# Kernel optimization log

Hardware: AMD Instinct MI355X
Metric: run time of the kernel (lower is better)

Reference implementation:

```python
import jax, jax.numpy as jnp
import numpy as np

B, N, K = 4, 100000, 128
Q_MIN = 0.5
S_B = 1.0
POT_SCALE = 1.0
REP_SCALE = 1.0
BETA_SCALE = 1.0
E_WEIGHT = 1.0
POS_WEIGHT = 1.0
TIME_WEIGHT = 1.0
HUBER_D = 2.0


def setup_inputs() -> dict:
    key = jax.random.key(0)
    ks = jax.random.split(key, 9)
    return {
        "beta": jax.random.uniform(ks[0], (B, N), dtype=jnp.float32),
        "ccoords": jax.random.normal(ks[1], (B, N, 2), dtype=jnp.float32),
        "pred_energy": jax.random.uniform(ks[2], (B, N), dtype=jnp.float32),
        "pred_pos": jax.random.normal(ks[3], (B, N, 2), dtype=jnp.float32),
        "pred_time": jax.random.uniform(ks[4], (B, N), dtype=jnp.float32),
        "t_energy": jax.random.uniform(ks[5], (B, N), dtype=jnp.float32),
        "t_pos": jax.random.normal(ks[6], (B, N, 2), dtype=jnp.float32),
        "t_time": jax.random.uniform(ks[7], (B, N), dtype=jnp.float32),
        "t_idx": jax.random.randint(ks[8], (B, N), 0, K + 1, dtype=jnp.int32),
    }


def _huber(x, d):
    a = jnp.abs(x)
    return jnp.where(a <= d, 0.5 * x * x, d * (a - 0.5 * d))


def _oc_loss(beta, ccoords, pred_energy, pred_pos, pred_time,
             t_energy, t_pos, t_time, t_idx):
    eps = 1e-4
    beta = jnp.clip(beta, eps, 1.0 - eps)
    q = jnp.arctanh(beta) ** 2 + Q_MIN                     # [B,N]

    obj = t_idx - 1                                        # -1 = noise, 0..K-1 = object id
    M = obj[:, :, None] == jnp.arange(K, dtype=jnp.int32)  # [B,N,K] bool membership
    Mf = M.astype(q.dtype)
    obj_exists = jnp.any(M, axis=1)                        # [B,K]
    exf = obj_exists.astype(q.dtype)

    # condensation point per object = member hit with max charge q (segment argmax)
    q_masked = jnp.where(M, q[:, :, None], -1.0)           # [B,N,K]
    alpha = jnp.argmax(q_masked, axis=1)                   # [B,K]
    x_alpha = jnp.take_along_axis(ccoords, alpha[:, :, None], axis=1)  # [B,K,2]
    q_alpha = jnp.take_along_axis(q, alpha, axis=1)        # [B,K]
    beta_alpha = jnp.take_along_axis(beta, alpha, axis=1)  # [B,K]

    # pairwise hit <-> condensation-point distances, [B,N,K]
    diff = ccoords[:, :, None, :] - x_alpha[:, None, :, :]
    dist = jnp.sqrt(jnp.sum(diff * diff, axis=-1) + 1e-12)

    qq = q[:, :, None] * q_alpha[:, None, :] * exf[:, None, :]
    v_att = qq * (dist * dist) * Mf
    v_rep = qq * jax.nn.relu(1.0 - dist) * (1.0 - Mf)
    n_tot = jnp.asarray(B * N, q.dtype)
    L_att = jnp.sum(v_att) / n_tot
    L_rep = jnp.sum(v_rep) / n_tot

    # beta loss: pull condensation-point betas to 1, suppress noise betas
    n_obj = jnp.maximum(jnp.sum(exf), 1.0)
    L_beta_obj = jnp.sum((1.0 - beta_alpha) * exf) / n_obj
    noise = (t_idx == 0).astype(q.dtype)
    L_noise = jnp.sum(beta * noise) / jnp.maximum(jnp.sum(noise), 1.0)
    L_beta = L_beta_obj + S_B * L_noise

    # payload losses, beta-weighted over non-noise hits
    p = (jnp.arctanh(beta) ** 2) * (1.0 - noise)           # [B,N]
    p_sum = jnp.maximum(jnp.sum(p), 1e-6)
    L_energy = jnp.sum(p * _huber(pred_energy - t_energy, HUBER_D)) / p_sum
    L_pos = jnp.sum(p * jnp.sum((pred_pos - t_pos) ** 2, axis=-1)) / p_sum
    L_time = jnp.sum(p * (pred_time - t_time) ** 2) / p_sum

    return (POT_SCALE * L_att + REP_SCALE * L_rep + BETA_SCALE * L_beta
            + E_WEIGHT * L_energy + POS_WEIGHT * L_pos + TIME_WEIGHT * L_time)


def reference(beta, ccoords, pred_energy, pred_pos, pred_time,
              t_energy, t_pos, t_time, t_idx):
    return _oc_loss(beta, ccoords, pred_energy, pred_pos, pred_time,
                    t_energy, t_pos, t_time, t_idx)
```

## Files before the change

kernel.cpp:

```cpp
#include <hip/hip_runtime.h>
#include <math.h>

#define BB 4
#define NN 100000
#define KK 128


__device__ __forceinline__ float clipb(float b) {
    return fminf(fmaxf(b, 1e-4f), 1.0f - 1e-4f);
}

__global__ void k_argmax(const float* __restrict__ beta,
                         const int* __restrict__ tidx,
                         unsigned long long* __restrict__ packed) {
    int b = blockIdx.y;
    __shared__ unsigned long long smax[KK];
    for (int t = threadIdx.x; t < KK; t += blockDim.x) smax[t] = 0ULL;
    __syncthreads();
    const float* betab = beta + b * NN;
    const int*   tib   = tidx + b * NN;
    for (int n = blockIdx.x * blockDim.x + threadIdx.x; n < NN;
         n += gridDim.x * blockDim.x) {
        int obj = tib[n] - 1;
        if (obj >= 0) {
            unsigned hi = __float_as_uint(clipb(betab[n]));
            unsigned long long key = ((unsigned long long)hi << 32) |
                                     (unsigned long long)(0xFFFFFFFFu - (unsigned)n);
            atomicMax(&smax[obj], key);
        }
    }
    __syncthreads();
    for (int t = threadIdx.x; t < KK; t += blockDim.x) {
        unsigned long long v = smax[t];
        if (v) atomicMax(&packed[b * KK + t], v);
    }
}

__global__ void k_gather(const unsigned long long* __restrict__ packed,
                         const float2* __restrict__ cc,
                         float4* __restrict__ sobj,
                         float* __restrict__ acc) {
    int t = blockIdx.x * blockDim.x + threadIdx.x;
    if (t >= BB * KK) return;
    int b = t / KK;
    unsigned long long v = packed[t];
    float4 o = make_float4(0.f, 0.f, 0.f, 0.f);
    if (v) {
        unsigned n = 0xFFFFFFFFu - (unsigned)(v & 0xFFFFFFFFu);
        float ba = __uint_as_float((unsigned)(v >> 32));
        float at = atanhf(ba);
        float2 c = cc[b * NN + (int)n];
        o.x = c.x; o.y = c.y; o.z = at * at + 0.5f; o.w = 1.0f;
        atomicAdd(&acc[8], 1.0f);
        atomicAdd(&acc[9], 1.0f - ba);
    }
    sobj[t] = o;
}

#define HH 2

__global__ void __launch_bounds__(256) k_main(
    const float*  __restrict__ beta, const float2* __restrict__ cc,
    const float*  __restrict__ pe,   const float2* __restrict__ pp,
    const float*  __restrict__ pt,   const float*  __restrict__ te,
    const float2* __restrict__ tp,   const float*  __restrict__ tt,
    const int*    __restrict__ tidx, const float4* __restrict__ sobjg,
    float* __restrict__ acc) {
    int b = blockIdx.y;
    __shared__ float4 sobj[KK];
    __shared__ float sred[4][8];
    for (int t = threadIdx.x; t < KK; t += blockDim.x) sobj[t] = sobjg[b * KK + t];
    __syncthreads();

    float p_att = 0.f, p_rep = 0.f, p_nb = 0.f, p_nc = 0.f;
    float p_ps = 0.f, p_e = 0.f, p_pos = 0.f, p_tm = 0.f;

    int n0 = blockIdx.x * (256 * HH) + threadIdx.x;
    int n1 = n0 + 256;
    bool v0 = n0 < NN, v1 = n1 < NN;
    int i0 = b * NN + (v0 ? n0 : 0);
    int i1 = b * NN + (v1 ? n1 : 0);

    float2 c0 = cc[i0], c1 = cc[i1];
    float rep0 = 0.f, rep1 = 0.f;

    #pragma unroll 8
    for (int k = 0; k < KK; ++k) {
        float4 o = sobj[k];
        float dx0 = c0.x - o.x, dy0 = c0.y - o.y;
        float dx1 = c1.x - o.x, dy1 = c1.y - o.y;
        float s0 = fmaf(dx0, dx0, fmaf(dy0, dy0, 1e-12f));
        float s1 = fmaf(dx1, dx1, fmaf(dy1, dy1, 1e-12f));
        float d0 = sqrtf(s0), d1 = sqrtf(s1);
        rep0 = fmaf(o.z, fmaxf(1.0f - d0, 0.0f), rep0);
        rep1 = fmaf(o.z, fmaxf(1.0f - d1, 0.0f), rep1);
    }

    #pragma unroll
    for (int h = 0; h < HH; ++h) {
        bool  vld = h ? v1 : v0;
        int   idx = h ? i1 : i0;
        float rep = h ? rep1 : rep0;
        float2 c  = h ? c1 : c0;
        if (!vld) continue;

        float bc  = clipb(beta[idx]);
        float at  = atanhf(bc);
        float at2 = at * at;
        float q   = at2 + 0.5f;
        int   ti  = tidx[idx];
        int   obj = ti - 1;

        if (obj >= 0) {
            float4 o = sobj[obj];
            float dx = c.x - o.x, dy = c.y - o.y;
            float s = fmaf(dx, dx, fmaf(dy, dy, 1e-12f));
            float d = sqrtf(s);
            rep   -= o.z * fmaxf(1.0f - d, 0.0f);
            p_att += q * (o.z * s);
        }
        p_rep += q * rep;

        if (ti == 0) {
            p_nb += bc;
            p_nc += 1.0f;
        } else {
            p_ps += at2;
            float de = pe[idx] - te[idx];
            float a  = fabsf(de);
            float hb = (a <= 2.0f) ? (0.5f * de * de) : (2.0f * (a - 1.0f));
            p_e  += at2 * hb;
            float2 ppv = pp[idx], tpv = tp[idx];
            float dpx = ppv.x - tpv.x, dpy = ppv.y - tpv.y;
            p_pos += at2 * (dpx * dpx + dpy * dpy);
            float dt = pt[idx] - tt[idx];
            p_tm += at2 * dt * dt;
        }
    }

    float vals[8] = {p_att, p_rep, p_nb, p_nc, p_ps, p_e, p_pos, p_tm};
    int lane = threadIdx.x & 63, wave = threadIdx.x >> 6;
    #pragma unroll
    for (int i = 0; i < 8; ++i) {
        float v = vals[i];
        for (int off = 32; off > 0; off >>= 1) v += __shfl_down(v, off, 64);
        if (lane == 0) sred[wave][i] = v;
    }
    __syncthreads();
    if (threadIdx.x < 8) {
        float s = sred[0][threadIdx.x] + sred[1][threadIdx.x] +
                  sred[2][threadIdx.x] + sred[3][threadIdx.x];
        atomicAdd(&acc[threadIdx.x], s);
    }
}

__global__ void k_final(const float* __restrict__ acc, float* __restrict__ out) {
    float inv_n  = 1.0f / (float)(BB * NN);
    float L_att  = acc[0] * inv_n;
    float L_rep  = acc[1] * inv_n;
    float n_obj  = fmaxf(acc[8], 1.0f);
    float L_beta = acc[9] / n_obj + acc[2] / fmaxf(acc[3], 1.0f);
    float p_sum  = fmaxf(acc[4], 1e-6f);
    out[0] = L_att + L_rep + L_beta + (acc[5] + acc[6] + acc[7]) / p_sum;
}

extern "C" void kernel_launch(void* const* d_in, const int* in_sizes, int n_in,
                              void* d_out, int out_size, void* d_ws, size_t ws_size,
                              hipStream_t stream) {
    const float*  beta = (const float*)d_in[0];
    const float2* cc   = (const float2*)d_in[1];
    const float*  pe   = (const float*)d_in[2];
    const float2* pp   = (const float2*)d_in[3];
    const float*  pt   = (const float*)d_in[4];
    const float*  te   = (const float*)d_in[5];
    const float2* tp   = (const float2*)d_in[6];
    const float*  tt   = (const float*)d_in[7];
    const int*    ti   = (const int*)d_in[8];

    unsigned long long* packed = (unsigned long long*)d_ws;
    float4* sobj = (float4*)((char*)d_ws + 4096);
    float*  acc  = (float*)((char*)d_ws + 12288);
    float*  out  = (float*)d_out;

    hipMemsetAsync(d_ws, 0, 12352, stream);

    k_argmax<<<dim3(64, BB), 256, 0, stream>>>(beta, ti, packed);
    k_gather<<<dim3(2), 256, 0, stream>>>(packed, cc, sobj, acc);
    k_main<<<dim3((NN + 256 * HH - 1) / (256 * HH), BB), 256, 0, stream>>>(
        beta, cc, pe, pp, pt, te, tp, tt, ti, sobj, acc);
    k_final<<<1, 1, 0, stream>>>(acc, out);
}
```

Before: 131.1 us.

## Prefetch per-hit inputs before K loop, use fast sqrt, replace atomics with partials

Per-hit loads in k_main (beta, tidx, payload and target arrays) are now issued before the shared-memory sync and the 128-object loop, so their memory latency overlaps the sobj fill and the distance computation. sqrtf is replaced with the hardware sqrt builtin. The global float atomics at the end of k_main are replaced by per-block partial sums, which a 64-thread k_final reduces. The argmax grid is doubled. The prefetch raises register pressure, and the builtin sqrt may differ slightly in precision from sqrtf.

```diff
diff --git a/kernel.cpp b/kernel.cpp
--- a/kernel.cpp
+++ b/kernel.cpp
@@ -4,6 +4,10 @@
 #define BB 4
 #define NN 100000
 #define KK 128
+#define HB 256
+#define HH 2
+#define GX ((NN + HB * HH - 1) / (HB * HH))
+#define NBLK (GX * BB)
 
 
 __device__ __forceinline__ float clipb(float b) {
@@ -57,33 +61,34 @@
     sobj[t] = o;
 }
 
-#define HH 2
-
-__global__ void __launch_bounds__(256) k_main(
+__global__ void __launch_bounds__(HB) k_main(
     const float*  __restrict__ beta, const float2* __restrict__ cc,
     const float*  __restrict__ pe,   const float2* __restrict__ pp,
     const float*  __restrict__ pt,   const float*  __restrict__ te,
     const float2* __restrict__ tp,   const float*  __restrict__ tt,
     const int*    __restrict__ tidx, const float4* __restrict__ sobjg,
-    float* __restrict__ acc) {
+    float* __restrict__ part) {
     int b = blockIdx.y;
     __shared__ float4 sobj[KK];
     __shared__ float sred[4][8];
-    for (int t = threadIdx.x; t < KK; t += blockDim.x) sobj[t] = sobjg[b * KK + t];
-    __syncthreads();
-
-    float p_att = 0.f, p_rep = 0.f, p_nb = 0.f, p_nc = 0.f;
-    float p_ps = 0.f, p_e = 0.f, p_pos = 0.f, p_tm = 0.f;
-
-    int n0 = blockIdx.x * (256 * HH) + threadIdx.x;
-    int n1 = n0 + 256;
+    for (int t = threadIdx.x; t < KK; t += HB) sobj[t] = sobjg[b * KK + t];
+
+    int n0 = blockIdx.x * (HB * HH) + threadIdx.x;
+    int n1 = n0 + HB;
     bool v0 = n0 < NN, v1 = n1 < NN;
     int i0 = b * NN + (v0 ? n0 : 0);
     int i1 = b * NN + (v1 ? n1 : 0);
 
-    float2 c0 = cc[i0], c1 = cc[i1];
+    float2 c0 = cc[i0],  c1 = cc[i1];
+    float bc0 = clipb(beta[i0]), bc1 = clipb(beta[i1]);
+    int   t0  = tidx[i0], t1 = tidx[i1];
+    float pe0 = pe[i0], pe1 = pe[i1], te0 = te[i0], te1 = te[i1];
+    float pt0 = pt[i0], pt1 = pt[i1], tt0 = tt[i0], tt1 = tt[i1];
+    float2 pp0 = pp[i0], pp1 = pp[i1], tp0 = tp[i0], tp1 = tp[i1];
+
+    __syncthreads();
+
     float rep0 = 0.f, rep1 = 0.f;
-
     #pragma unroll 8
     for (int k = 0; k < KK; ++k) {
         float4 o = sobj[k];
@@ -91,31 +96,32 @@
         float dx1 = c1.x - o.x, dy1 = c1.y - o.y;
         float s0 = fmaf(dx0, dx0, fmaf(dy0, dy0, 1e-12f));
         float s1 = fmaf(dx1, dx1, fmaf(dy1, dy1, 1e-12f));
-        float d0 = sqrtf(s0), d1 = sqrtf(s1);
+        float d0 = __builtin_amdgcn_sqrtf(s0);
+        float d1 = __builtin_amdgcn_sqrtf(s1);
         rep0 = fmaf(o.z, fmaxf(1.0f - d0, 0.0f), rep0);
         rep1 = fmaf(o.z, fmaxf(1.0f - d1, 0.0f), rep1);
     }
 
+    float p_att = 0.f, p_rep = 0.f, p_nb = 0.f, p_nc = 0.f;
+    float p_ps = 0.f, p_e = 0.f, p_pos = 0.f, p_tm = 0.f;
+
     #pragma unroll
     for (int h = 0; h < HH; ++h) {
-        bool  vld = h ? v1 : v0;
-        int   idx = h ? i1 : i0;
+        bool  vld = h ? v1 : v0;   if (!vld) continue;
         float rep = h ? rep1 : rep0;
         float2 c  = h ? c1 : c0;
-        if (!vld) continue;
-
-        float bc  = clipb(beta[idx]);
+        float bc  = h ? bc1 : bc0;
+        int   ti  = h ? t1 : t0;
         float at  = atanhf(bc);
         float at2 = at * at;
         float q   = at2 + 0.5f;
-        int   ti  = tidx[idx];
         int   obj = ti - 1;
 
         if (obj >= 0) {
             float4 o = sobj[obj];
             float dx = c.x - o.x, dy = c.y - o.y;
             float s = fmaf(dx, dx, fmaf(dy, dy, 1e-12f));
-            float d = sqrtf(s);
+            float d = __builtin_amdgcn_sqrtf(s);
             rep   -= o.z * fmaxf(1.0f - d, 0.0f);
             p_att += q * (o.z * s);
         }
@@ -126,14 +132,14 @@
             p_nc += 1.0f;
         } else {
             p_ps += at2;
-            float de = pe[idx] - te[idx];
+            float de = (h ? pe1 : pe0) - (h ? te1 : te0);
             float a  = fabsf(de);
             float hb = (a <= 2.0f) ? (0.5f * de * de) : (2.0f * (a - 1.0f));
             p_e  += at2 * hb;
-            float2 ppv = pp[idx], tpv = tp[idx];
+            float2 ppv = h ? pp1 : pp0, tpv = h ? tp1 : tp0;
             float dpx = ppv.x - tpv.x, dpy = ppv.y - tpv.y;
             p_pos += at2 * (dpx * dpx + dpy * dpy);
-            float dt = pt[idx] - tt[idx];
+            float dt = (h ? pt1 : pt0) - (h ? tt1 : tt0);
             p_tm += at2 * dt * dt;
         }
     }
@@ -143,6 +149,7 @@
     #pragma unroll
     for (int i = 0; i < 8; ++i) {
         float v = vals[i];
+        #pragma unroll
         for (int off = 32; off > 0; off >>= 1) v += __shfl_down(v, off, 64);
         if (lane == 0) sred[wave][i] = v;
     }
@@ -150,18 +157,33 @@
     if (threadIdx.x < 8) {
         float s = sred[0][threadIdx.x] + sred[1][threadIdx.x] +
                   sred[2][threadIdx.x] + sred[3][threadIdx.x];
-        atomicAdd(&acc[threadIdx.x], s);
-    }
-}
-
-__global__ void k_final(const float* __restrict__ acc, float* __restrict__ out) {
-    float inv_n  = 1.0f / (float)(BB * NN);
-    float L_att  = acc[0] * inv_n;
-    float L_rep  = acc[1] * inv_n;
-    float n_obj  = fmaxf(acc[8], 1.0f);
-    float L_beta = acc[9] / n_obj + acc[2] / fmaxf(acc[3], 1.0f);
-    float p_sum  = fmaxf(acc[4], 1e-6f);
-    out[0] = L_att + L_rep + L_beta + (acc[5] + acc[6] + acc[7]) / p_sum;
+        int bid = b * GX + blockIdx.x;
+        part[bid * 8 + threadIdx.x] = s;
+    }
+}
+
+__global__ void __launch_bounds__(64) k_final(const float* __restrict__ part,
+                                              const float* __restrict__ acc,
+                                              float* __restrict__ out) {
+    int lane = threadIdx.x;
+    int comp = lane & 7;
+    float v = 0.f;
+    for (int r = lane >> 3; r < NBLK; r += 8)
+        v += part[r * 8 + comp];
+    v += __shfl_xor(v, 8, 64);
+    v += __shfl_xor(v, 16, 64);
+    v += __shfl_xor(v, 32, 64);
+    float tot[8];
+    #pragma unroll
+    for (int c = 0; c < 8; ++c) tot[c] = __shfl(v, c, 64);
+    if (lane == 0) {
+        float inv_n  = 1.0f / (float)(BB * NN);
+        float n_obj  = fmaxf(acc[8], 1.0f);
+        float L_beta = acc[9] / n_obj + tot[2] / fmaxf(tot[3], 1.0f);
+        float p_sum  = fmaxf(tot[4], 1e-6f);
+        out[0] = tot[0] * inv_n + tot[1] * inv_n + L_beta +
+                 (tot[5] + tot[6] + tot[7]) / p_sum;
+    }
 }
 
 extern "C" void kernel_launch(void* const* d_in, const int* in_sizes, int n_in,
@@ -180,13 +202,14 @@
     unsigned long long* packed = (unsigned long long*)d_ws;
     float4* sobj = (float4*)((char*)d_ws + 4096);
     float*  acc  = (float*)((char*)d_ws + 12288);
+    float*  part = (float*)((char*)d_ws + 12416);
     float*  out  = (float*)d_out;
 
     hipMemsetAsync(d_ws, 0, 12352, stream);
 
-    k_argmax<<<dim3(64, BB), 256, 0, stream>>>(beta, ti, packed);
+    k_argmax<<<dim3(128, BB), 256, 0, stream>>>(beta, ti, packed);
     k_gather<<<dim3(2), 256, 0, stream>>>(packed, cc, sobj, acc);
-    k_main<<<dim3((NN + 256 * HH - 1) / (256 * HH), BB), 256, 0, stream>>>(
-        beta, cc, pe, pp, pt, te, tp, tt, ti, sobj, acc);
-    k_final<<<1, 1, 0, stream>>>(acc, out);
-}
+    k_main<<<dim3(GX, BB), HB, 0, stream>>>(
+        beta, cc, pe, pp, pt, te, tp, tt, ti, sobj, part);
+    k_final<<<1, 64, 0, stream>>>(part, acc, out);
+}
```

New measurement: 135.1 us. 3.1% more time.
